# Optimization experiments

Measured on AMD Instinct MI355X. Metric: run time of the kernel, lower is better.

The kernel has to match this reference:

```python
import jax, jax.numpy as jnp
import numpy as np

N = 50000
E = 800000
IN_DIM = 512
HID = 64
OUT = 64
HEADS = 4
NEG_SLOPE = 0.2


def setup_inputs() -> dict:
    key = jax.random.key(0)
    ks = jax.random.split(key, 16)
    s = 0.05
    inp = {
        "x": jax.random.normal(ks[0], (N, IN_DIM), jnp.float32),
        "edge_index": jax.random.randint(ks[1], (2, E), 0, N, jnp.int64),
        # layer 1: in=512 -> heads*hid = 4*64 = 256, concat=True
        "W1l": jax.random.normal(ks[2], (IN_DIM, HEADS * HID), jnp.float32) * s,
        "b1l": jnp.zeros((HEADS * HID,), jnp.float32),
        "W1r": jax.random.normal(ks[3], (IN_DIM, HEADS * HID), jnp.float32) * s,
        "b1r": jnp.zeros((HEADS * HID,), jnp.float32),
        "att1": jax.random.normal(ks[4], (HEADS, HID), jnp.float32) * s,
        "bias1": jnp.zeros((HEADS * HID,), jnp.float32),
        # layer 2: in=256 -> heads*(2*out) = 4*128, concat=False (mean heads)
        "W2l": jax.random.normal(ks[5], (HEADS * HID, HEADS * 2 * OUT), jnp.float32) * s,
        "b2l": jnp.zeros((HEADS * 2 * OUT,), jnp.float32),
        "W2r": jax.random.normal(ks[6], (HEADS * HID, HEADS * 2 * OUT), jnp.float32) * s,
        "b2r": jnp.zeros((HEADS * 2 * OUT,), jnp.float32),
        "att2": jax.random.normal(ks[7], (HEADS, 2 * OUT), jnp.float32) * s,
        "bias2": jnp.zeros((2 * OUT,), jnp.float32),
    }
    return inp


def _gatv2(x, src, dst, Wl, bl, Wr, br, att, bias, concat):
    """GATv2Conv (PyG semantics): message x_l[src], attention over incoming edges per dst."""
    H, C = att.shape
    n = x.shape[0]
    xl = (x @ Wl + bl).reshape(n, H, C)  # source transform (messages)
    xr = (x @ Wr + br).reshape(n, H, C)  # target transform
    g = jax.nn.leaky_relu(xl[src] + xr[dst], NEG_SLOPE)   # [E, H, C]
    e = jnp.einsum('ehc,hc->eh', g, att)                  # [E, H]
    # numerically-stable softmax over irregular neighbor sets (segmented by dst)
    m = jax.ops.segment_max(e, dst, num_segments=n)
    ex = jnp.exp(e - m[dst])
    denom = jax.ops.segment_sum(ex, dst, num_segments=n)
    alpha = ex / (denom[dst] + 1e-16)                     # [E, H]
    out = jax.ops.segment_sum(xl[src] * alpha[..., None], dst, num_segments=n)  # [N, H, C]
    if concat:
        return out.reshape(n, H * C) + bias
    return out.mean(axis=1) + bias


def reference(x, edge_index, W1l, b1l, W1r, b1r, att1, bias1,
              W2l, b2l, W2r, b2r, att2, bias2):
    # add self loops (PyG add_self_loops=True default)
    loops = jnp.arange(N, dtype=edge_index.dtype)
    src = jnp.concatenate([edge_index[0], loops])
    dst = jnp.concatenate([edge_index[1], loops])
    h = jax.nn.relu(_gatv2(x, src, dst, W1l, b1l, W1r, b1r, att1, bias1, concat=True))
    return _gatv2(h, src, dst, W2l, b2l, W2r, b2r, att2, bias2, concat=False)
```

## Files before the change

### kernel.cpp

```cpp
#include <hip/hip_runtime.h>

#define NNODES 50000
#define NEDGES 800000
#define ET (NEDGES + NNODES)
#define HEADS 4

typedef __attribute__((ext_vector_type(8))) short bf16x8;
typedef __attribute__((ext_vector_type(4))) float f32x4;

#define EXP2F(x) __builtin_amdgcn_exp2f(x)

#define GLOAD16(g, l) __builtin_amdgcn_global_load_lds(                      \
    (const __attribute__((address_space(1))) unsigned int*)(g),              \
    (__attribute__((address_space(3))) unsigned int*)(l), 16, 0, 0)

__device__ inline unsigned short f2bf(float f) {
  union { float f; unsigned int i; } c; c.f = f;
  unsigned int b = c.i + 0x7fffu + ((c.i >> 16) & 1u);
  return (unsigned short)(b >> 16);
}
__device__ inline float4 b4tof(uint2 r) {
  float4 f;
  union { unsigned int i; float v; } c;
  c.i = r.x << 16;          f.x = c.v;
  c.i = r.x & 0xffff0000u;  f.y = c.v;
  c.i = r.y << 16;          f.z = c.v;
  c.i = r.y & 0xffff0000u;  f.w = c.v;
  return f;
}


__global__ void k_hist(const int* __restrict__ ei, int* __restrict__ deg) {
  int i = blockIdx.x * blockDim.x + threadIdx.x;
  if (i >= ET) return;
  int dst = (i < NEDGES) ? ei[NEDGES + i] : (i - NEDGES);
  atomicAdd(&deg[dst], 1);
}

__global__ void k_scan1(const int* __restrict__ deg, int* __restrict__ part,
                        int* __restrict__ bsum, int n) {
  __shared__ int s[256];
  int tid = threadIdx.x;
  int i = blockIdx.x * 256 + tid;
  int v = (i < n) ? deg[i] : 0;
  s[tid] = v;
  __syncthreads();
  for (int off = 1; off < 256; off <<= 1) {
    int t = (tid >= off) ? s[tid - off] : 0;
    __syncthreads();
    s[tid] += t;
    __syncthreads();
  }
  if (i < n) part[i] = s[tid] - v;
  if (tid == 255) bsum[blockIdx.x] = s[255];
}

__global__ void k_scan2(int* bsum, int nb) {
  __shared__ int s[256];
  int t = threadIdx.x;
  int v = (t < nb) ? bsum[t] : 0;
  s[t] = v;
  __syncthreads();
  for (int off = 1; off < 256; off <<= 1) {
    int tv = (t >= off) ? s[t - off] : 0;
    __syncthreads();
    s[t] += tv;
    __syncthreads();
  }
  if (t < nb) bsum[t] = s[t] - v;
}

__global__ void k_scan3(const int* __restrict__ part, const int* __restrict__ bsum,
                        int* __restrict__ rowstart, int* __restrict__ cursor,
                        int n, int total) {
  int i = blockIdx.x * blockDim.x + threadIdx.x;
  if (i < n) {
    int v = part[i] + bsum[i >> 8];
    rowstart[i] = v;
    cursor[i] = v;
  }
  if (i == n) rowstart[n] = total;
}

__global__ void k_scatter(const int* __restrict__ ei, int* __restrict__ cursor,
                          int* __restrict__ csrsrc) {
  int i = blockIdx.x * blockDim.x + threadIdx.x;
  if (i >= ET) return;
  int src, dst;
  if (i < NEDGES) { src = ei[i]; dst = ei[NEDGES + i]; }
  else            { src = dst = i - NEDGES; }
  int pos = atomicAdd(&cursor[dst], 1);
  csrsrc[pos] = src;
}


__global__ void k_cast_bf16(const float* __restrict__ in, unsigned short* __restrict__ out, int n4) {
  int i = blockIdx.x * blockDim.x + threadIdx.x;
  if (i >= n4) return;
  float4 v = ((const float4*)in)[i];
  ushort4 o;
  o.x = f2bf(v.x); o.y = f2bf(v.y); o.z = f2bf(v.z); o.w = f2bf(v.w);
  ((ushort4*)out)[i] = o;
}

__global__ __launch_bounds__(256) void k_castw_all(
    const float* __restrict__ W1l, const float* __restrict__ W1r,
    const float* __restrict__ W2l, const float* __restrict__ W2r,
    unsigned short* __restrict__ w1t, unsigned short* __restrict__ w2t) {
  __shared__ float tile[32][33];
  int which = blockIdx.y;
  const float* W;
  unsigned short* T;
  int K, N, noff;
  if (which == 0)      { W = W1l; T = w1t; K = 512; N = 256; noff = 0; }
  else if (which == 1) { W = W1r; T = w1t; K = 512; N = 256; noff = 256; }
  else if (which == 2) { W = W2l; T = w2t; K = 256; N = 512; noff = 0; }
  else                 { W = W2r; T = w2t; K = 256; N = 512; noff = 512; }
  int tpr = N >> 5;
  int tk = (blockIdx.x / tpr) << 5;
  int tn = (blockIdx.x % tpr) << 5;
  int c = threadIdx.x & 31, r = threadIdx.x >> 5;
#pragma unroll
  for (int rr = 0; rr < 32; rr += 8)
    tile[r + rr][c] = W[(size_t)(tk + r + rr) * N + tn + c];
  __syncthreads();
#pragma unroll
  for (int rr = 0; rr < 32; rr += 8)
    T[(size_t)(tn + r + rr + noff) * K + tk + c] = f2bf(tile[c][r + rr]);
}


__global__ __launch_bounds__(256) void k_gemm(
    const unsigned short* __restrict__ A, const unsigned short* __restrict__ Bt,
    const float* __restrict__ bL, const float* __restrict__ bR, int nsplit,
    unsigned short* __restrict__ C, int M, int K, int N) {
  __shared__ unsigned short As[2][128 * 32];
  __shared__ unsigned short Bs[2][128 * 32];
  int tid = threadIdx.x;
  int lane = tid & 63, wave = tid >> 6;
  int wr = (wave >> 1) * 64, wc = (wave & 1) * 64;
  int row0 = blockIdx.x * 128, col0 = blockIdx.y * 128;
  int fr = lane & 15, fq = lane >> 4;
  int sr = tid >> 2, sc = (tid & 3) * 8;

  const unsigned short* ga0 = &A[(size_t)(row0 + sr) * K + sc];
  const unsigned short* ga1 = &A[(size_t)(row0 + sr + 64) * K + sc];
  const unsigned short* gb0 = &Bt[(size_t)(col0 + sr) * K + sc];
  const unsigned short* gb1 = &Bt[(size_t)(col0 + sr + 64) * K + sc];

  f32x4 acc[4][4] = {};
  const int NT = K >> 5;

  GLOAD16(ga0, &As[0][tid * 8]);
  GLOAD16(ga1, &As[0][2048 + tid * 8]);
  GLOAD16(gb0, &Bs[0][tid * 8]);
  GLOAD16(gb1, &Bs[0][2048 + tid * 8]);
  asm volatile("s_waitcnt vmcnt(0)" ::: "memory");
  __builtin_amdgcn_s_barrier();

  int cur = 0;
  for (int t = 0; t < NT; ++t) {
    if (t + 1 < NT) {
      int k0 = (t + 1) << 5;
      GLOAD16(ga0 + k0, &As[cur ^ 1][tid * 8]);
      GLOAD16(ga1 + k0, &As[cur ^ 1][2048 + tid * 8]);
      GLOAD16(gb0 + k0, &Bs[cur ^ 1][tid * 8]);
      GLOAD16(gb1 + k0, &Bs[cur ^ 1][2048 + tid * 8]);
    }
    bf16x8 af[4], bfr[4];
#pragma unroll
    for (int m = 0; m < 4; ++m)
      af[m] = *(const bf16x8*)&As[cur][(wr + m * 16 + fr) * 32 + fq * 8];
#pragma unroll
    for (int n = 0; n < 4; ++n)
      bfr[n] = *(const bf16x8*)&Bs[cur][(wc + n * 16 + fr) * 32 + fq * 8];
#pragma unroll
    for (int m = 0; m < 4; ++m)
#pragma unroll
      for (int n = 0; n < 4; ++n)
        acc[m][n] = __builtin_amdgcn_mfma_f32_16x16x32_bf16(af[m], bfr[n], acc[m][n], 0, 0, 0);
    asm volatile("s_waitcnt vmcnt(0)" ::: "memory");
    __builtin_amdgcn_s_barrier();
    cur ^= 1;
  }

#pragma unroll
  for (int m = 0; m < 4; ++m) {
#pragma unroll
    for (int n = 0; n < 4; ++n) {
      int col = col0 + wc + n * 16 + fr;
      float bv = (col < nsplit) ? bL[col] : bR[col - nsplit];
#pragma unroll
      for (int j = 0; j < 4; ++j) {
        int row = row0 + wr + m * 16 + fq * 4 + j;
        if (row < M) C[(size_t)row * N + col] = f2bf(acc[m][n][j] + bv);
      }
    }
  }
}


template <int CQ>
__device__ inline void load_row(const unsigned short* p, float4* xv) {
  if constexpr (CQ == 1) {
    xv[0] = b4tof(*(const uint2*)p);
  } else {
    uint4 r = *(const uint4*)p;
    xv[0] = b4tof(make_uint2(r.x, r.y));
    xv[1] = b4tof(make_uint2(r.z, r.w));
  }
}

template <int CQ>
__device__ inline float edge_score(const float4* xv, const float4* xrv, const float4* attv) {
  float p = 0.f;
#pragma unroll
  for (int q = 0; q < CQ; ++q) {
    float s;
    s = xv[q].x + xrv[q].x; p = fmaf(attv[q].x, fmaxf(s, 0.2f * s), p);
    s = xv[q].y + xrv[q].y; p = fmaf(attv[q].y, fmaxf(s, 0.2f * s), p);
    s = xv[q].z + xrv[q].z; p = fmaf(attv[q].z, fmaxf(s, 0.2f * s), p);
    s = xv[q].w + xrv[q].w; p = fmaf(attv[q].w, fmaxf(s, 0.2f * s), p);
  }
  return p;
}

template <int CQ, int MODE, int STR>
__global__ __launch_bounds__(256) void k_fused(
    const int* __restrict__ rowstart, const int* __restrict__ csrsrc,
    const unsigned short* __restrict__ xlr,
    const float* __restrict__ att, const float* __restrict__ bias,
    void* __restrict__ outp) {
  const int C = CQ * 64;
  const int CHL = CQ * 4;
  int dst = (blockIdx.x * blockDim.x + threadIdx.x) >> 6;
  int lane = threadIdx.x & 63;
  if (dst >= NNODES) return;
  int h = lane >> 4;
  int l = lane & 15;
  const int choff = h * C + l * CHL;

  float4 xrv[CQ], attv[CQ];
  load_row<CQ>(&xlr[(size_t)dst * STR + STR / 2 + choff], xrv);
#pragma unroll
  for (int q = 0; q < CQ; ++q) {
    float4 a = *(const float4*)&att[choff + q * 4];
    a.x *= 1.44269504f; a.y *= 1.44269504f;
    a.z *= 1.44269504f; a.w *= 1.44269504f;
    attv[q] = a;
  }

  int rs = __builtin_amdgcn_readfirstlane(rowstart[dst]);
  int re = __builtin_amdgcn_readfirstlane(rowstart[dst + 1]);

  float den = 0.f;
  float4 acc[CQ];
#pragma unroll
  for (int q = 0; q < CQ; ++q) acc[q] = make_float4(0.f, 0.f, 0.f, 0.f);

  int i = rs;
  for (; i + 4 <= re; i += 4) {
    int s0 = csrsrc[i + 0];
    int s1 = csrsrc[i + 1];
    int s2 = csrsrc[i + 2];
    int s3 = csrsrc[i + 3];
    float4 x0[CQ], x1[CQ], x2[CQ], x3[CQ];
    load_row<CQ>(&xlr[(unsigned)s0 * (unsigned)STR + choff], x0);
    load_row<CQ>(&xlr[(unsigned)s1 * (unsigned)STR + choff], x1);
    load_row<CQ>(&xlr[(unsigned)s2 * (unsigned)STR + choff], x2);
    load_row<CQ>(&xlr[(unsigned)s3 * (unsigned)STR + choff], x3);
    float p0 = edge_score<CQ>(x0, xrv, attv);
    float p1 = edge_score<CQ>(x1, xrv, attv);
    float p2 = edge_score<CQ>(x2, xrv, attv);
    float p3 = edge_score<CQ>(x3, xrv, attv);
#pragma unroll
    for (int d = 1; d <= 8; d <<= 1) {
      p0 += __shfl_xor(p0, d);
      p1 += __shfl_xor(p1, d);
      p2 += __shfl_xor(p2, d);
      p3 += __shfl_xor(p3, d);
    }
    float w0 = EXP2F(p0), w1 = EXP2F(p1), w2 = EXP2F(p2), w3 = EXP2F(p3);
    den += (w0 + w1) + (w2 + w3);
#pragma unroll
    for (int q = 0; q < CQ; ++q) {
      acc[q].x = fmaf(w0, x0[q].x, fmaf(w1, x1[q].x, fmaf(w2, x2[q].x, fmaf(w3, x3[q].x, acc[q].x))));
      acc[q].y = fmaf(w0, x0[q].y, fmaf(w1, x1[q].y, fmaf(w2, x2[q].y, fmaf(w3, x3[q].y, acc[q].y))));
      acc[q].z = fmaf(w0, x0[q].z, fmaf(w1, x1[q].z, fmaf(w2, x2[q].z, fmaf(w3, x3[q].z, acc[q].z))));
      acc[q].w = fmaf(w0, x0[q].w, fmaf(w1, x1[q].w, fmaf(w2, x2[q].w, fmaf(w3, x3[q].w, acc[q].w))));
    }
  }
  for (; i < re; ++i) {
    int s0 = csrsrc[i];
    float4 x0[CQ];
    load_row<CQ>(&xlr[(unsigned)s0 * (unsigned)STR + choff], x0);
    float p0 = edge_score<CQ>(x0, xrv, attv);
#pragma unroll
    for (int d = 1; d <= 8; d <<= 1) p0 += __shfl_xor(p0, d);
    float w0 = EXP2F(p0);
    den += w0;
#pragma unroll
    for (int q = 0; q < CQ; ++q) {
      acc[q].x = fmaf(w0, x0[q].x, acc[q].x);
      acc[q].y = fmaf(w0, x0[q].y, acc[q].y);
      acc[q].z = fmaf(w0, x0[q].z, acc[q].z);
      acc[q].w = fmaf(w0, x0[q].w, acc[q].w);
    }
  }

  float inv = 1.f / (den + 1e-16f);

  if (MODE == 0) {
    unsigned short* out = (unsigned short*)outp;
#pragma unroll
    for (int q = 0; q < CQ; ++q) {
      const float4 bv = *(const float4*)&bias[choff + q * 4];
      ushort4 o;
      o.x = f2bf(fmaxf(acc[q].x * inv + bv.x, 0.f));
      o.y = f2bf(fmaxf(acc[q].y * inv + bv.y, 0.f));
      o.z = f2bf(fmaxf(acc[q].z * inv + bv.z, 0.f));
      o.w = f2bf(fmaxf(acc[q].w * inv + bv.w, 0.f));
      *(ushort4*)&out[(size_t)dst * (HEADS * C) + choff + q * 4] = o;
    }
  } else {
    float* out = (float*)outp;
    float r[CQ][4];
#pragma unroll
    for (int q = 0; q < CQ; ++q) {
      r[q][0] = acc[q].x * inv; r[q][1] = acc[q].y * inv;
      r[q][2] = acc[q].z * inv; r[q][3] = acc[q].w * inv;
    }
#pragma unroll
    for (int q = 0; q < CQ; ++q)
#pragma unroll
      for (int j = 0; j < 4; ++j) {
        r[q][j] += __shfl_xor(r[q][j], 16);
        r[q][j] += __shfl_xor(r[q][j], 32);
      }
    if (lane < 16) {
#pragma unroll
      for (int q = 0; q < CQ; ++q) {
        int c = lane * CHL + q * 4;
        float4 o;
        o.x = r[q][0] * 0.25f + bias[c + 0];
        o.y = r[q][1] * 0.25f + bias[c + 1];
        o.z = r[q][2] * 0.25f + bias[c + 2];
        o.w = r[q][3] * 0.25f + bias[c + 3];
        *(float4*)&out[(size_t)dst * C + c] = o;
      }
    }
  }
}


extern "C" void kernel_launch(void* const* d_in, const int* in_sizes, int n_in,
                              void* d_out, int out_size, void* d_ws, size_t ws_size,
                              hipStream_t stream) {
  (void)in_sizes; (void)n_in; (void)out_size; (void)ws_size;
  const float* x     = (const float*)d_in[0];
  const int*   ei    = (const int*)d_in[1];
  const float* W1l   = (const float*)d_in[2];
  const float* b1l   = (const float*)d_in[3];
  const float* W1r   = (const float*)d_in[4];
  const float* b1r   = (const float*)d_in[5];
  const float* att1  = (const float*)d_in[6];
  const float* bias1 = (const float*)d_in[7];
  const float* W2l   = (const float*)d_in[8];
  const float* b2l   = (const float*)d_in[9];
  const float* W2r   = (const float*)d_in[10];
  const float* b2r   = (const float*)d_in[11];
  const float* att2  = (const float*)d_in[12];
  const float* bias2 = (const float*)d_in[13];
  float* out = (float*)d_out;

  char* ws = (char*)d_ws;
  size_t off = 0;
  auto alloc = [&](size_t bytes) {
    char* p = ws + off;
    off = (off + bytes + 255) & ~(size_t)255;
    return p;
  };
  int*  deg      = (int*)alloc((size_t)NNODES * 4);
  int*  part     = (int*)alloc((size_t)NNODES * 4);
  int*  bsum     = (int*)alloc(256 * 4);
  int*  rowstart = (int*)alloc((size_t)(NNODES + 1) * 4);
  int*  cursor   = (int*)alloc((size_t)NNODES * 4);
  int*  csrsrc   = (int*)alloc((size_t)ET * 4);
  unsigned short* xb   = (unsigned short*)alloc((size_t)NNODES * 512 * 2);
  unsigned short* w1t  = (unsigned short*)alloc((size_t)512 * 512 * 2);
  unsigned short* w2t  = (unsigned short*)alloc((size_t)1024 * 256 * 2);
  unsigned short* xlr1 = (unsigned short*)alloc((size_t)NNODES * 512 * 2);
  unsigned short* hbuf = (unsigned short*)alloc((size_t)NNODES * 256 * 2);
  unsigned short* xlr2 = (unsigned short*)alloc((size_t)NNODES * 1024 * 2);
  (void)alloc(64 * 1024);

  (void)hipMemsetAsync(deg, 0, (size_t)NNODES * 4, stream);
  k_hist<<<(ET + 255) / 256, 256, 0, stream>>>(ei, deg);
  int nb = (NNODES + 255) / 256;
  k_scan1<<<nb, 256, 0, stream>>>(deg, part, bsum, NNODES);
  k_scan2<<<1, 256, 0, stream>>>(bsum, nb);
  k_scan3<<<(NNODES + 256) / 256, 256, 0, stream>>>(part, bsum, rowstart, cursor, NNODES, ET);
  k_scatter<<<(ET + 255) / 256, 256, 0, stream>>>(ei, cursor, csrsrc);

  k_cast_bf16<<<(NNODES * 512 / 4 + 255) / 256, 256, 0, stream>>>(x, xb, NNODES * 512 / 4);
  k_castw_all<<<dim3(128, 4), 256, 0, stream>>>(W1l, W1r, W2l, W2r, w1t, w2t);

  const int gridM = (NNODES + 127) / 128;
  const int gridFused = (NNODES + 3) / 4;

  k_gemm<<<dim3(gridM, 4), 256, 0, stream>>>(xb, w1t, b1l, b1r, 256, xlr1, NNODES, 512, 512);
  k_fused<1, 0, 512><<<gridFused, 256, 0, stream>>>(rowstart, csrsrc, xlr1, att1, bias1, hbuf);

  k_gemm<<<dim3(gridM, 8), 256, 0, stream>>>(hbuf, w2t, b2l, b2r, 512, xlr2, NNODES, 256, 1024);
  k_fused<2, 1, 1024><<<gridFused, 256, 0, stream>>>(rowstart, csrsrc, xlr2, att2, bias2, out);
}
```

Measured before the change: 468.1 us.

## Triple-buffer GEMM loads and software-pipeline packed-math edge aggregation

```diff
diff --git a/kernel.cpp b/kernel.cpp
--- a/kernel.cpp
+++ b/kernel.cpp
@@ -7,8 +7,21 @@
 
 typedef __attribute__((ext_vector_type(8))) short bf16x8;
 typedef __attribute__((ext_vector_type(4))) float f32x4;
+typedef __attribute__((ext_vector_type(2))) float f32x2v;
 
 #define EXP2F(x) __builtin_amdgcn_exp2f(x)
+
+#if defined(__has_builtin)
+#if __has_builtin(__builtin_elementwise_fma)
+#define VFMA(a, b, c) __builtin_elementwise_fma((a), (b), (c))
+#endif
+#endif
+#ifndef VFMA
+__device__ inline f32x2v vfma_(f32x2v a, f32x2v b, f32x2v c) {
+  f32x2v r; r.x = fmaf(a.x, b.x, c.x); r.y = fmaf(a.y, b.y, c.y); return r;
+}
+#define VFMA vfma_
+#endif
 
 #define GLOAD16(g, l) __builtin_amdgcn_global_load_lds(                      \
     (const __attribute__((address_space(1))) unsigned int*)(g),              \
@@ -19,14 +32,14 @@
   unsigned int b = c.i + 0x7fffu + ((c.i >> 16) & 1u);
   return (unsigned short)(b >> 16);
 }
-__device__ inline float4 b4tof(uint2 r) {
-  float4 f;
-  union { unsigned int i; float v; } c;
-  c.i = r.x << 16;          f.x = c.v;
-  c.i = r.x & 0xffff0000u;  f.y = c.v;
-  c.i = r.y << 16;          f.z = c.v;
-  c.i = r.y & 0xffff0000u;  f.w = c.v;
-  return f;
+__device__ inline f32x2v cvtpair(unsigned u) {
+  union { unsigned i; float f; } lo, hi;
+  lo.i = u << 16; hi.i = u & 0xffff0000u;
+  f32x2v r; r.x = lo.f; r.y = hi.f; return r;
+}
+__device__ inline f32x2v vabs2(f32x2v s) {
+  union { f32x2v f; unsigned u[2]; } c; c.f = s;
+  c.u[0] &= 0x7fffffffu; c.u[1] &= 0x7fffffffu; return c.f;
 }
 
 
@@ -130,12 +143,18 @@
 }
 
 
+template <int N> __device__ __forceinline__ void waitvm() {
+  if constexpr (N == 0) asm volatile("s_waitcnt vmcnt(0)" ::: "memory");
+  else if constexpr (N == 4) asm volatile("s_waitcnt vmcnt(4)" ::: "memory");
+  else asm volatile("s_waitcnt vmcnt(8)" ::: "memory");
+}
+
 __global__ __launch_bounds__(256) void k_gemm(
     const unsigned short* __restrict__ A, const unsigned short* __restrict__ Bt,
     const float* __restrict__ bL, const float* __restrict__ bR, int nsplit,
     unsigned short* __restrict__ C, int M, int K, int N) {
-  __shared__ unsigned short As[2][128 * 32];
-  __shared__ unsigned short Bs[2][128 * 32];
+  __shared__ unsigned short As[3][128 * 32];
+  __shared__ unsigned short Bs[3][128 * 32];
   int tid = threadIdx.x;
   int lane = tid & 63, wave = tid >> 6;
   int wr = (wave >> 1) * 64, wc = (wave & 1) * 64;
@@ -151,38 +170,50 @@
   f32x4 acc[4][4] = {};
   const int NT = K >> 5;
 
-  GLOAD16(ga0, &As[0][tid * 8]);
-  GLOAD16(ga1, &As[0][2048 + tid * 8]);
-  GLOAD16(gb0, &Bs[0][tid * 8]);
-  GLOAD16(gb1, &Bs[0][2048 + tid * 8]);
-  asm volatile("s_waitcnt vmcnt(0)" ::: "memory");
-  __builtin_amdgcn_s_barrier();
-
-  int cur = 0;
-  for (int t = 0; t < NT; ++t) {
-    if (t + 1 < NT) {
-      int k0 = (t + 1) << 5;
-      GLOAD16(ga0 + k0, &As[cur ^ 1][tid * 8]);
-      GLOAD16(ga1 + k0, &As[cur ^ 1][2048 + tid * 8]);
-      GLOAD16(gb0 + k0, &Bs[cur ^ 1][tid * 8]);
-      GLOAD16(gb1 + k0, &Bs[cur ^ 1][2048 + tid * 8]);
-    }
-    bf16x8 af[4], bfr[4];
-#pragma unroll
-    for (int m = 0; m < 4; ++m)
-      af[m] = *(const bf16x8*)&As[cur][(wr + m * 16 + fr) * 32 + fq * 8];
-#pragma unroll
-    for (int n = 0; n < 4; ++n)
-      bfr[n] = *(const bf16x8*)&Bs[cur][(wc + n * 16 + fr) * 32 + fq * 8];
-#pragma unroll
-    for (int m = 0; m < 4; ++m)
-#pragma unroll
-      for (int n = 0; n < 4; ++n)
-        acc[m][n] = __builtin_amdgcn_mfma_f32_16x16x32_bf16(af[m], bfr[n], acc[m][n], 0, 0, 0);
-    asm volatile("s_waitcnt vmcnt(0)" ::: "memory");
+#define STAGE(b, k0)                                  \
+  do {                                                \
+    GLOAD16(ga0 + (k0), &As[b][tid * 8]);             \
+    GLOAD16(ga1 + (k0), &As[b][2048 + tid * 8]);      \
+    GLOAD16(gb0 + (k0), &Bs[b][tid * 8]);             \
+    GLOAD16(gb1 + (k0), &Bs[b][2048 + tid * 8]);      \
+  } while (0)
+
+#define COMPUTE(b)                                                        \
+  do {                                                                    \
+    bf16x8 af[4], bfr[4];                                                 \
+    _Pragma("unroll")                                                     \
+    for (int m = 0; m < 4; ++m)                                           \
+      af[m] = *(const bf16x8*)&As[b][(wr + m * 16 + fr) * 32 + fq * 8];   \
+    _Pragma("unroll")                                                     \
+    for (int n = 0; n < 4; ++n)                                           \
+      bfr[n] = *(const bf16x8*)&Bs[b][(wc + n * 16 + fr) * 32 + fq * 8];  \
+    _Pragma("unroll")                                                     \
+    for (int m = 0; m < 4; ++m)                                           \
+      _Pragma("unroll")                                                   \
+      for (int n = 0; n < 4; ++n)                                         \
+        acc[m][n] = __builtin_amdgcn_mfma_f32_16x16x32_bf16(af[m], bfr[n], acc[m][n], 0, 0, 0); \
+  } while (0)
+
+  STAGE(0, 0);
+  STAGE(1, 32);
+  STAGE(2, 64);
+
+  for (int t = 0; t < NT - 3; ++t) {
+    int b = t % 3;
+    waitvm<8>();
     __builtin_amdgcn_s_barrier();
-    cur ^= 1;
-  }
+    COMPUTE(b);
+    asm volatile("s_waitcnt lgkmcnt(0)" ::: "memory");
+    __builtin_amdgcn_sched_barrier(0);
+    __builtin_amdgcn_s_barrier();
+    STAGE(b, (t + 3) << 5);
+  }
+  waitvm<8>(); __builtin_amdgcn_s_barrier(); COMPUTE((NT - 3) % 3);
+  waitvm<4>(); __builtin_amdgcn_s_barrier(); COMPUTE((NT - 2) % 3);
+  waitvm<0>(); __builtin_amdgcn_s_barrier(); COMPUTE((NT - 1) % 3);
+
+#undef STAGE
+#undef COMPUTE
 
 #pragma unroll
   for (int m = 0; m < 4; ++m) {
@@ -200,29 +231,14 @@
 }
 
 
+template <int CQ> struct raw_t;
+template <> struct raw_t<1> { using T = uint2; };
+template <> struct raw_t<2> { using T = uint4; };
+
 template <int CQ>
-__device__ inline void load_row(const unsigned short* p, float4* xv) {
-  if constexpr (CQ == 1) {
-    xv[0] = b4tof(*(const uint2*)p);
-  } else {
-    uint4 r = *(const uint4*)p;
-    xv[0] = b4tof(make_uint2(r.x, r.y));
-    xv[1] = b4tof(make_uint2(r.z, r.w));
-  }
-}
-
-template <int CQ>
-__device__ inline float edge_score(const float4* xv, const float4* xrv, const float4* attv) {
-  float p = 0.f;
-#pragma unroll
-  for (int q = 0; q < CQ; ++q) {
-    float s;
-    s = xv[q].x + xrv[q].x; p = fmaf(attv[q].x, fmaxf(s, 0.2f * s), p);
-    s = xv[q].y + xrv[q].y; p = fmaf(attv[q].y, fmaxf(s, 0.2f * s), p);
-    s = xv[q].z + xrv[q].z; p = fmaf(attv[q].z, fmaxf(s, 0.2f * s), p);
-    s = xv[q].w + xrv[q].w; p = fmaf(attv[q].w, fmaxf(s, 0.2f * s), p);
-  }
-  return p;
+__device__ __forceinline__ void rawwords(const typename raw_t<CQ>::T& r, unsigned* u) {
+  u[0] = r.x; u[1] = r.y;
+  if constexpr (CQ == 2) { u[2] = r.z; u[3] = r.w; }
 }
 
 template <int CQ, int MODE, int STR>
@@ -233,6 +249,8 @@
     void* __restrict__ outp) {
   const int C = CQ * 64;
   const int CHL = CQ * 4;
+  const int P = CQ * 2;
+  using RawT = typename raw_t<CQ>::T;
   int dst = (blockIdx.x * blockDim.x + threadIdx.x) >> 6;
   int lane = threadIdx.x & 63;
   if (dst >= NNODES) return;
@@ -240,39 +258,58 @@
   int l = lane & 15;
   const int choff = h * C + l * CHL;
 
-  float4 xrv[CQ], attv[CQ];
-  load_row<CQ>(&xlr[(size_t)dst * STR + STR / 2 + choff], xrv);
-#pragma unroll
-  for (int q = 0; q < CQ; ++q) {
-    float4 a = *(const float4*)&att[choff + q * 4];
-    a.x *= 1.44269504f; a.y *= 1.44269504f;
-    a.z *= 1.44269504f; a.w *= 1.44269504f;
-    attv[q] = a;
-  }
+  f32x2v xr2[P], a04[P];
+  {
+    RawT xrr = *(const RawT*)&xlr[(size_t)dst * STR + STR / 2 + choff];
+    unsigned u[4];
+    rawwords<CQ>(xrr, u);
+#pragma unroll
+    for (int j = 0; j < P; ++j) {
+      xr2[j] = cvtpair(u[j]);
+      a04[j].x = att[choff + j * 2 + 0] * (0.4f * 1.44269504f);
+      a04[j].y = att[choff + j * 2 + 1] * (0.4f * 1.44269504f);
+    }
+  }
+  const f32x2v c15 = {1.5f, 1.5f};
 
   int rs = __builtin_amdgcn_readfirstlane(rowstart[dst]);
   int re = __builtin_amdgcn_readfirstlane(rowstart[dst + 1]);
 
   float den = 0.f;
-  float4 acc[CQ];
-#pragma unroll
-  for (int q = 0; q < CQ; ++q) acc[q] = make_float4(0.f, 0.f, 0.f, 0.f);
-
-  int i = rs;
-  for (; i + 4 <= re; i += 4) {
-    int s0 = csrsrc[i + 0];
-    int s1 = csrsrc[i + 1];
-    int s2 = csrsrc[i + 2];
-    int s3 = csrsrc[i + 3];
-    float4 x0[CQ], x1[CQ], x2[CQ], x3[CQ];
-    load_row<CQ>(&xlr[(unsigned)s0 * (unsigned)STR + choff], x0);
-    load_row<CQ>(&xlr[(unsigned)s1 * (unsigned)STR + choff], x1);
-    load_row<CQ>(&xlr[(unsigned)s2 * (unsigned)STR + choff], x2);
-    load_row<CQ>(&xlr[(unsigned)s3 * (unsigned)STR + choff], x3);
-    float p0 = edge_score<CQ>(x0, xrv, attv);
-    float p1 = edge_score<CQ>(x1, xrv, attv);
-    float p2 = edge_score<CQ>(x2, xrv, attv);
-    float p3 = edge_score<CQ>(x3, xrv, attv);
+  f32x2v acc2[P];
+#pragma unroll
+  for (int j = 0; j < P; ++j) acc2[j] = (f32x2v){0.f, 0.f};
+
+  auto score = [&](const RawT& r) -> float {
+    unsigned u[4];
+    rawwords<CQ>(r, u);
+    f32x2v p2 = {0.f, 0.f};
+#pragma unroll
+    for (int j = 0; j < P; ++j) {
+      f32x2v x2 = cvtpair(u[j]);
+      f32x2v s = x2 + xr2[j];
+      f32x2v inner = VFMA(c15, s, vabs2(s));
+      p2 = VFMA(a04[j], inner, p2);
+    }
+    return p2.x + p2.y;
+  };
+
+  auto load4 = [&](RawT& r0, RawT& r1, RawT& r2, RawT& r3, int idx) {
+    int s0 = csrsrc[idx + 0];
+    int s1 = csrsrc[idx + 1];
+    int s2 = csrsrc[idx + 2];
+    int s3 = csrsrc[idx + 3];
+    r0 = *(const RawT*)&xlr[(unsigned)s0 * (unsigned)STR + choff];
+    r1 = *(const RawT*)&xlr[(unsigned)s1 * (unsigned)STR + choff];
+    r2 = *(const RawT*)&xlr[(unsigned)s2 * (unsigned)STR + choff];
+    r3 = *(const RawT*)&xlr[(unsigned)s3 * (unsigned)STR + choff];
+  };
+
+  auto consume4 = [&](const RawT& r0, const RawT& r1, const RawT& r2, const RawT& r3) {
+    float p0 = score(r0);
+    float p1 = score(r1);
+    float p2 = score(r2);
+    float p3 = score(r3);
 #pragma unroll
     for (int d = 1; d <= 8; d <<= 1) {
       p0 += __shfl_xor(p0, d);
@@ -282,30 +319,48 @@
     }
     float w0 = EXP2F(p0), w1 = EXP2F(p1), w2 = EXP2F(p2), w3 = EXP2F(p3);
     den += (w0 + w1) + (w2 + w3);
-#pragma unroll
-    for (int q = 0; q < CQ; ++q) {
-      acc[q].x = fmaf(w0, x0[q].x, fmaf(w1, x1[q].x, fmaf(w2, x2[q].x, fmaf(w3, x3[q].x, acc[q].x))));
-      acc[q].y = fmaf(w0, x0[q].y, fmaf(w1, x1[q].y, fmaf(w2, x2[q].y, fmaf(w3, x3[q].y, acc[q].y))));
-      acc[q].z = fmaf(w0, x0[q].z, fmaf(w1, x1[q].z, fmaf(w2, x2[q].z, fmaf(w3, x3[q].z, acc[q].z))));
-      acc[q].w = fmaf(w0, x0[q].w, fmaf(w1, x1[q].w, fmaf(w2, x2[q].w, fmaf(w3, x3[q].w, acc[q].w))));
-    }
+    f32x2v w0v = {w0, w0}, w1v = {w1, w1}, w2v = {w2, w2}, w3v = {w3, w3};
+    unsigned u0[4], u1[4], u2[4], u3[4];
+    rawwords<CQ>(r0, u0); rawwords<CQ>(r1, u1);
+    rawwords<CQ>(r2, u2); rawwords<CQ>(r3, u3);
+#pragma unroll
+    for (int j = 0; j < P; ++j) {
+      f32x2v a = acc2[j];
+      a = VFMA(w0v, cvtpair(u0[j]), a);
+      a = VFMA(w1v, cvtpair(u1[j]), a);
+      a = VFMA(w2v, cvtpair(u2[j]), a);
+      a = VFMA(w3v, cvtpair(u3[j]), a);
+      acc2[j] = a;
+    }
+  };
+
+  int nb = (re - rs) >> 2;
+  int i = rs;
+  if (nb > 0) {
+    RawT A0, A1, A2, A3, B0, B1, B2, B3;
+    load4(A0, A1, A2, A3, i);
+    for (int b = 1; b < nb; ++b) {
+      if (b & 1) { load4(B0, B1, B2, B3, i + 4); consume4(A0, A1, A2, A3); }
+      else       { load4(A0, A1, A2, A3, i + 4); consume4(B0, B1, B2, B3); }
+      i += 4;
+    }
+    if (nb & 1) consume4(A0, A1, A2, A3);
+    else        consume4(B0, B1, B2, B3);
+    i += 4;
   }
   for (; i < re; ++i) {
     int s0 = csrsrc[i];
-    float4 x0[CQ];
-    load_row<CQ>(&xlr[(unsigned)s0 * (unsigned)STR + choff], x0);
-    float p0 = edge_score<CQ>(x0, xrv, attv);
+    RawT r0 = *(const RawT*)&xlr[(unsigned)s0 * (unsigned)STR + choff];
+    float p0 = score(r0);
 #pragma unroll
     for (int d = 1; d <= 8; d <<= 1) p0 += __shfl_xor(p0, d);
     float w0 = EXP2F(p0);
     den += w0;
-#pragma unroll
-    for (int q = 0; q < CQ; ++q) {
-      acc[q].x = fmaf(w0, x0[q].x, acc[q].x);
-      acc[q].y = fmaf(w0, x0[q].y, acc[q].y);
-      acc[q].z = fmaf(w0, x0[q].z, acc[q].z);
-      acc[q].w = fmaf(w0, x0[q].w, acc[q].w);
-    }
+    f32x2v wv = {w0, w0};
+    unsigned u[4];
+    rawwords<CQ>(r0, u);
+#pragma unroll
+    for (int j = 0; j < P; ++j) acc2[j] = VFMA(wv, cvtpair(u[j]), acc2[j]);
   }
 
   float inv = 1.f / (den + 1e-16f);
@@ -316,36 +371,34 @@
     for (int q = 0; q < CQ; ++q) {
       const float4 bv = *(const float4*)&bias[choff + q * 4];
       ushort4 o;
-      o.x = f2bf(fmaxf(acc[q].x * inv + bv.x, 0.f));
-      o.y = f2bf(fmaxf(acc[q].y * inv + bv.y, 0.f));
-      o.z = f2bf(fmaxf(acc[q].z * inv + bv.z, 0.f));
-      o.w = f2bf(fmaxf(acc[q].w * inv + bv.w, 0.f));
+      o.x = f2bf(fmaxf(acc2[q * 2 + 0].x * inv + bv.x, 0.f));
+      o.y = f2bf(fmaxf(acc2[q * 2 + 0].y * inv + bv.y, 0.f));
+      o.z = f2bf(fmaxf(acc2[q * 2 + 1].x * inv + bv.z, 0.f));
+      o.w = f2bf(fmaxf(acc2[q * 2 + 1].y * inv + bv.w, 0.f));
       *(ushort4*)&out[(size_t)dst * (HEADS * C) + choff + q * 4] = o;
     }
   } else {
     float* out = (float*)outp;
-    float r[CQ][4];
-#pragma unroll
-    for (int q = 0; q < CQ; ++q) {
-      r[q][0] = acc[q].x * inv; r[q][1] = acc[q].y * inv;
-      r[q][2] = acc[q].z * inv; r[q][3] = acc[q].w * inv;
-    }
-#pragma unroll
-    for (int q = 0; q < CQ; ++q)
-#pragma unroll
-      for (int j = 0; j < 4; ++j) {
-        r[q][j] += __shfl_xor(r[q][j], 16);
-        r[q][j] += __shfl_xor(r[q][j], 32);
-      }
+    float rr[8];
+#pragma unroll
+    for (int j = 0; j < P; ++j) {
+      rr[j * 2 + 0] = acc2[j].x * inv;
+      rr[j * 2 + 1] = acc2[j].y * inv;
+    }
+#pragma unroll
+    for (int c = 0; c < CHL; ++c) {
+      rr[c] += __shfl_xor(rr[c], 16);
+      rr[c] += __shfl_xor(rr[c], 32);
+    }
     if (lane < 16) {
 #pragma unroll
       for (int q = 0; q < CQ; ++q) {
         int c = lane * CHL + q * 4;
         float4 o;
-        o.x = r[q][0] * 0.25f + bias[c + 0];
-        o.y = r[q][1] * 0.25f + bias[c + 1];
-        o.z = r[q][2] * 0.25f + bias[c + 2];
-        o.w = r[q][3] * 0.25f + bias[c + 3];
+        o.x = rr[q * 4 + 0] * 0.25f + bias[c + 0];
+        o.y = rr[q * 4 + 1] * 0.25f + bias[c + 1];
+        o.z = rr[q * 4 + 2] * 0.25f + bias[c + 2];
+        o.w = rr[q * 4 + 3] * 0.25f + bias[c + 3];
         *(float4*)&out[(size_t)dst * C + c] = o;
       }
     }
```

New measurement: 463.7 us. Within noise of the previous version (-0.9%).
